# Optimization experiments

Hardware: AMD Instinct MI355X
Metric: run time of the kernel (lower is better)

Reference implementation:

```python
import jax, jax.numpy as jnp
import numpy as np

MAX_DISP = 48
N, C, H, W = 4, 32, 256, 512

def setup_inputs() -> dict:
    key = jax.random.key(0)
    k1, k2 = jax.random.split(key)
    l_fmap = jax.random.normal(k1, (N, C, H, W), dtype=jnp.float32)
    r_fmap = jax.random.normal(k2, (N, C, H, W), dtype=jnp.float32)
    return {"l_fmap": l_fmap, "r_fmap": r_fmap, "use_naive": 1}

def _cost_volume(l_fmap, r_fmap):
    # cost[n, d, h, w] = mean_c l[n,c,h,w] * r[n,c,h,w-d], zero where w < d
    n, c, h, w = l_fmap.shape
    items = []
    for d in range(MAX_DISP):
        if d == 0:
            r_shift = r_fmap
        else:
            # shift right by d with zero padding on the left (columns w<d -> 0)
            r_shift = jnp.pad(r_fmap[..., : w - d], ((0, 0), (0, 0), (0, 0), (d, 0)))
        items.append(jnp.mean(l_fmap * r_shift, axis=1))  # [n, h, w]
    return jnp.stack(items, axis=1)  # [n, max_disp, h, w]

def reference(l_fmap, r_fmap, use_naive):
    # naive and conv2d paths compute identical math; use_naive is ignored
    return _cost_volume(l_fmap, r_fmap)
```

## Files before the change

### kernel.cpp

```cpp
#include <hip/hip_runtime.h>

#define CC 32
#define HH 256
#define WW 512
#define NN 4
#define MAXD 48

#define WT 256
#define RW (WT + MAXD)
#define DTILE 12
#define WTILE 4

__global__ __launch_bounds__(256, 4)
void cost_volume_kernel(const float* __restrict__ L,
                        const float* __restrict__ R,
                        float* __restrict__ out)
{
    __shared__ float r_s[CC][RW];

    const int t  = threadIdx.x;
    const int w0 = blockIdx.x * WT;
    const int h  = blockIdx.y;
    const int n  = blockIdx.z;

    const size_t chw  = (size_t)HH * WW;
    const size_t rowB = (size_t)n * CC * chw + (size_t)h * WW;

    #pragma unroll
    for (int k = 0; k < 10; ++k) {
        int idx = t + 256 * k;
        if (idx < 2432) {
            int c   = idx / 76;
            int j4  = idx - c * 76;
            int g   = w0 - MAXD + 4 * j4;
            float4 v = make_float4(0.f, 0.f, 0.f, 0.f);
            if (g >= 0)
                v = *(const float4*)(R + rowB + (size_t)c * chw + g);
            *(float4*)&r_s[c][4 * j4] = v;
        }
    }
    __syncthreads();

    const int wg = t & 63;
    const int dg = t >> 6;
    const int wb = wg * WTILE;
    const int d0 = dg * DTILE;
    const int jA = wb + 36 - d0;

    float acc[DTILE][WTILE];
    #pragma unroll
    for (int k = 0; k < DTILE; ++k)
        #pragma unroll
        for (int i = 0; i < WTILE; ++i)
            acc[k][i] = 0.f;

    const float* lp = L + rowB + w0 + wb;
    float4 lv0 = *(const float4*)(lp);
    float4 lv1 = *(const float4*)(lp + chw);
    for (int c = 0; c < CC; ++c) {
        float4 lnext;
        if (c + 2 < CC)
            lnext = *(const float4*)(lp + (size_t)(c + 2) * chw);
        float rv[16];
        #pragma unroll
        for (int q = 0; q < 4; ++q)
            *(float4*)&rv[4 * q] = *(const float4*)&r_s[c][jA + 4 * q];
        const float lf[4] = {lv0.x, lv0.y, lv0.z, lv0.w};
        #pragma unroll
        for (int k = 0; k < DTILE; ++k)
            #pragma unroll
            for (int i = 0; i < WTILE; ++i)
                acc[k][i] += lf[i] * rv[12 + i - k];
        lv0 = lv1;
        lv1 = lnext;
    }

    const float inv = 1.0f / 32.0f;
    #pragma unroll
    for (int k = 0; k < DTILE; ++k) {
        const int d = d0 + k;
        float4 o = make_float4(acc[k][0] * inv, acc[k][1] * inv,
                               acc[k][2] * inv, acc[k][3] * inv);
        *(float4*)(out + (((size_t)n * MAXD + d) * HH + h) * WW + w0 + wb) = o;
    }
}

extern "C" void kernel_launch(void* const* d_in, const int* in_sizes, int n_in,
                              void* d_out, int out_size, void* d_ws, size_t ws_size,
                              hipStream_t stream) {
    const float* L = (const float*)d_in[0];
    const float* R = (const float*)d_in[1];
    float* out = (float*)d_out;
    dim3 grid(WW / WT, HH, NN);
    cost_volume_kernel<<<grid, dim3(256, 1, 1), 0, stream>>>(L, R, out);
}
```

Baseline: 211.5 us.

## Stream R rows per wave via async global-to-LDS loads with pipelined waits

Replaces the block-wide preload of all 32 R channels into shared memory, which needed a __syncthreads, with per-wave 4-slot ring buffers. Each wave fills its own buffer using global_load_lds (direct global-to-LDS) three channels ahead, along with the L loads, and uses manual vmcnt waits instead of a barrier. This overlaps memory latency with the FMA work and shrinks LDS use, which may allow more blocks per CU. The cost is that each of the four waves fetches R redundantly, and the hand-counted vmcnt values and sched barriers are fragile.

```diff
diff --git a/kernel.cpp b/kernel.cpp
--- a/kernel.cpp
+++ b/kernel.cpp
@@ -16,34 +16,19 @@
                         const float* __restrict__ R,
                         float* __restrict__ out)
 {
-    __shared__ float r_s[CC][RW];
+    __shared__ float r_s[4][4][RW];
 
-    const int t  = threadIdx.x;
-    const int w0 = blockIdx.x * WT;
-    const int h  = blockIdx.y;
-    const int n  = blockIdx.z;
+    const int t    = threadIdx.x;
+    const int lane = t & 63;
+    const int dg   = t >> 6;
+    const int w0   = blockIdx.x * WT;
+    const int h    = blockIdx.y;
+    const int n    = blockIdx.z;
 
     const size_t chw  = (size_t)HH * WW;
     const size_t rowB = (size_t)n * CC * chw + (size_t)h * WW;
 
-    #pragma unroll
-    for (int k = 0; k < 10; ++k) {
-        int idx = t + 256 * k;
-        if (idx < 2432) {
-            int c   = idx / 76;
-            int j4  = idx - c * 76;
-            int g   = w0 - MAXD + 4 * j4;
-            float4 v = make_float4(0.f, 0.f, 0.f, 0.f);
-            if (g >= 0)
-                v = *(const float4*)(R + rowB + (size_t)c * chw + g);
-            *(float4*)&r_s[c][4 * j4] = v;
-        }
-    }
-    __syncthreads();
-
-    const int wg = t & 63;
-    const int dg = t >> 6;
-    const int wb = wg * WTILE;
+    const int wb = lane * WTILE;
     const int d0 = dg * DTILE;
     const int jA = wb + 36 - d0;
 
@@ -54,26 +39,77 @@
         for (int i = 0; i < WTILE; ++i)
             acc[k][i] = 0.f;
 
-    const float* lp = L + rowB + w0 + wb;
-    float4 lv0 = *(const float4*)(lp);
-    float4 lv1 = *(const float4*)(lp + chw);
-    for (int c = 0; c < CC; ++c) {
-        float4 lnext;
-        if (c + 2 < CC)
-            lnext = *(const float4*)(lp + (size_t)(c + 2) * chw);
-        float rv[16];
+    if (w0 == 0 && lane < 12) {
         #pragma unroll
-        for (int q = 0; q < 4; ++q)
-            *(float4*)&rv[4 * q] = *(const float4*)&r_s[c][jA + 4 * q];
-        const float lf[4] = {lv0.x, lv0.y, lv0.z, lv0.w};
-        #pragma unroll
-        for (int k = 0; k < DTILE; ++k)
-            #pragma unroll
-            for (int i = 0; i < WTILE; ++i)
-                acc[k][i] += lf[i] * rv[12 + i - k];
-        lv0 = lv1;
-        lv1 = lnext;
+        for (int b = 0; b < 4; ++b)
+            *(float4*)&r_s[dg][b][4 * lane] = make_float4(0.f, 0.f, 0.f, 0.f);
     }
+
+    const int   fullR = (w0 != 0);
+    const float* Rbase = R + rowB + w0 - MAXD;
+    const float* lp    = L + rowB + w0 + wb;
+
+#define ISSUE(s) do {                                                         \
+        const float* rb = Rbase + (size_t)(s) * chw;                          \
+        float* lb = &r_s[dg][(s) & 3][0];                                     \
+        if (fullR | (lane >= 12))                                             \
+            __builtin_amdgcn_global_load_lds(                                 \
+                (const __attribute__((address_space(1))) void*)(rb + 4*lane), \
+                (__attribute__((address_space(3))) void*)lb, 16, 0, 0);       \
+        if (lane < 12)                                                        \
+            __builtin_amdgcn_global_load_lds(                                 \
+                (const __attribute__((address_space(1))) void*)(rb + 256 + 4*lane), \
+                (__attribute__((address_space(3))) void*)(lb + 256), 16, 0, 0); \
+    } while (0)
+
+#define WAITN(nv) asm volatile("s_waitcnt vmcnt(" #nv ")" ::: "memory")
+#define SCHED0()  __builtin_amdgcn_sched_barrier(0)
+
+    float4 lv[4];
+    lv[0] = *(const float4*)(lp);
+    ISSUE(0); SCHED0();
+    lv[1] = *(const float4*)(lp + chw);
+    ISSUE(1); SCHED0();
+    lv[2] = *(const float4*)(lp + 2 * chw);
+    ISSUE(2); SCHED0();
+
+#define STEP(c, W) do {                                                       \
+        if ((c) + 3 < CC) {                                                   \
+            lv[((c) + 3) & 3] = *(const float4*)(lp + (size_t)((c)+3) * chw); \
+            ISSUE((c) + 3);                                                   \
+        }                                                                     \
+        WAITN(W);                                                             \
+        {                                                                     \
+            float rv[16];                                                     \
+            const float* rs = &r_s[dg][(c) & 3][jA];                          \
+            *(float4*)&rv[0]  = *(const float4*)(rs);                         \
+            *(float4*)&rv[4]  = *(const float4*)(rs + 4);                     \
+            *(float4*)&rv[8]  = *(const float4*)(rs + 8);                     \
+            *(float4*)&rv[12] = *(const float4*)(rs + 12);                    \
+            const float4 lf = lv[(c) & 3];                                    \
+            _Pragma("unroll")                                                 \
+            for (int k = 0; k < DTILE; ++k) {                                 \
+                acc[k][0] += lf.x * rv[12 - k];   \
+                acc[k][1] += lf.y * rv[13 - k];                               \
+                acc[k][2] += lf.z * rv[14 - k];                               \
+                acc[k][3] += lf.w * rv[15 - k];                               \
+            }                                                                 \
+        }                                                                     \
+        SCHED0();                                                             \
+    } while (0)
+
+    STEP( 0, 9); STEP( 1, 9); STEP( 2, 9); STEP( 3, 9); STEP( 4, 9);
+    STEP( 5, 9); STEP( 6, 9); STEP( 7, 9); STEP( 8, 9); STEP( 9, 9);
+    STEP(10, 9); STEP(11, 9); STEP(12, 9); STEP(13, 9); STEP(14, 9);
+    STEP(15, 9); STEP(16, 9); STEP(17, 9); STEP(18, 9); STEP(19, 9);
+    STEP(20, 9); STEP(21, 9); STEP(22, 9); STEP(23, 9); STEP(24, 9);
+    STEP(25, 9); STEP(26, 9); STEP(27, 9); STEP(28, 9);
+    STEP(29, 6); STEP(30, 3); STEP(31, 0);
+
+#undef STEP
+#undef ISSUE
+#undef WAITN
+#undef SCHED0
 
     const float inv = 1.0f / 32.0f;
     #pragma unroll
```

Result: slower. 743.8 us (+251.8%).
